# Optimization experiments

Measured on AMD Instinct MI355X. Metric: run time of the kernel, lower is better.

## Reference

```python
import jax, jax.numpy as jnp
import numpy as np

NUM_CLASSES = 21
NEGPOS_RATIO = 3
B, P = 64, 24564


def setup_inputs() -> dict:
    key = jax.random.key(0)
    ks = jax.random.split(key, 10)
    return {
        "loc_data": jax.random.normal(ks[0], (B, P, 4), jnp.float32),
        "conf_data": jax.random.normal(ks[1], (B, P, NUM_CLASSES), jnp.float32),
        "has_lp_data": jax.random.normal(ks[2], (B, P, 2), jnp.float32),
        "size_lp_data": jax.random.normal(ks[3], (B, P, 2), jnp.float32),
        "offset_data": jax.random.normal(ks[4], (B, P, 2), jnp.float32),
        "loc_t": jax.random.normal(ks[5], (B, P, 4), jnp.float32),
        "conf_t": jax.random.randint(ks[6], (B, P), 0, NUM_CLASSES, jnp.int64),
        "has_lp_t": jax.random.randint(ks[7], (B, P), 0, 2, jnp.int64),
        "size_lp_t": jax.random.normal(ks[8], (B, P, 2), jnp.float32),
        "offset_t": jax.random.normal(ks[9], (B, P, 2), jnp.float32),
    }


def _smooth_l1_sum(p, t, mask):
    # sum-reduced smooth L1 (beta=1) over elements selected by mask
    d = jnp.abs(p - t)
    l = jnp.where(d < 1.0, 0.5 * d * d, d - 0.5)
    return jnp.sum(l * mask)


def _ce_per_row(logits, labels):
    # per-row cross entropy: logsumexp(logits) - logits[label]
    lse = jax.nn.logsumexp(logits, axis=-1)
    g = jnp.take_along_axis(logits, labels[..., None], axis=-1)[..., 0]
    return lse - g


def reference(loc_data, conf_data, has_lp_data, size_lp_data, offset_data,
              loc_t, conf_t, has_lp_t, size_lp_t, offset_t):
    dt = loc_data.dtype
    num_priors = conf_data.shape[1]
    pos = conf_t > 0                                  # [B,P]
    posf = pos.astype(dt)[..., None]                  # [B,P,1]

    # localization loss over positives
    loss_l = _smooth_l1_sum(loc_data, loc_t, posf)

    # size / offset losses over positives, gated by has_lp flag
    hlp = has_lp_t.astype(dt)[..., None]              # [B,P,1]
    loss_size_lp = _smooth_l1_sum(size_lp_data * hlp, size_lp_t * hlp, posf)
    loss_offset = _smooth_l1_sum(offset_data * hlp, offset_t * hlp, posf)

    # hard negative mining on per-prior conf CE
    ce = _ce_per_row(conf_data, conf_t)               # [B,P]
    ce_mine = jnp.where(pos, 0.0, ce)
    loss_idx = jnp.argsort(-ce_mine, axis=1)          # descending sort indices
    idx_rank = jnp.argsort(loss_idx, axis=1)          # rank of each prior
    num_pos = jnp.sum(pos, axis=1, keepdims=True)     # [B,1]
    num_neg = jnp.clip(NEGPOS_RATIO * num_pos, None, num_priors - 1)
    neg = idx_rank < num_neg                          # [B,P]
    sel = (pos | neg).astype(dt)

    loss_c = jnp.sum(ce * sel)
    loss_has_lp = jnp.sum(_ce_per_row(has_lp_data, has_lp_t) * sel)

    N = jnp.sum(pos).astype(dt)
    return (loss_l / N, loss_c / N, loss_size_lp / N,
            loss_offset / N, loss_has_lp / N)
```

## Files before the change

### kernel.cpp

```cpp
#include <hip/hip_runtime.h>
#include <stdint.h>

#define NC 21
#define BATCH 64
#define PRI 24564
#define NROWS (BATCH * PRI)
#define SLABS 32
#define SLABR 768
#define GBLK (BATCH * SLABS)

typedef float f4a4 __attribute__((ext_vector_type(4), aligned(4)));

__device__ __forceinline__ float sl1f(float p, float t) {
    float d = fabsf(p - t);
    return d < 1.0f ? 0.5f * d * d : d - 0.5f;
}

__device__ __forceinline__ unsigned int f2k(float v) {
    unsigned int u = __float_as_uint(v);
    return (u & 0x80000000u) ? ~u : (u | 0x80000000u);
}

__device__ __forceinline__ unsigned int chkey(float2 ch) {
    unsigned hb = __float_as_uint(ch.y);
    return (hb & 0x80000000u) ? 0x80000000u : f2k(ch.x);
}

__device__ __forceinline__ double blockReduce(double v, double* sred) {
    #pragma unroll
    for (int off = 32; off > 0; off >>= 1)
        v += __shfl_down(v, off, 64);
    const int wid = threadIdx.x >> 6, lane = threadIdx.x & 63;
    __syncthreads();
    if (lane == 0) sred[wid] = v;
    __syncthreads();
    double r = 0.0;
    if (threadIdx.x == 0) r = sred[0] + sred[1] + sred[2] + sred[3];
    return r;
}

__global__ __launch_bounds__(256) void k_main(
    const float* __restrict__ loc_data, const float* __restrict__ conf_data,
    const float* __restrict__ has_lp_data, const float* __restrict__ size_lp_data,
    const float* __restrict__ offset_data, const float* __restrict__ loc_t,
    const int* __restrict__ conf_t, const int* __restrict__ has_lp_t,
    const float* __restrict__ size_lp_t, const float* __restrict__ offset_t,
    float2* __restrict__ ws_ch, int* __restrict__ numpos, double* __restrict__ part,
    int* __restrict__ ghist1)
{
    __shared__ int hist[4096];
    __shared__ double sred[4];
    const int tid = threadIdx.x;
    const int b = blockIdx.x >> 5, s = blockIdx.x & 31;
    for (int k = tid; k < 4096; k += 256) hist[k] = 0;
    __syncthreads();

    double aL = 0.0, aS = 0.0, aO = 0.0;
    int myp = 0;

    #pragma unroll
    for (int i = 0; i < 3; ++i) {
        const int p = s * SLABR + i * 256 + tid;
        if (p < PRI) {
            const unsigned r = (unsigned)b * PRI + p;
            const int c = conf_t[r];
            const bool pos = c > 0;
            const int hl = has_lp_t[r];

            const float* crow = conf_data + (long)r * NC;
            const f4a4* cr4 = (const f4a4*)crow;
            float row[NC];
            #pragma unroll
            for (int j = 0; j < 5; ++j) {
                f4a4 v = cr4[j];
                row[4*j+0] = v.x; row[4*j+1] = v.y; row[4*j+2] = v.z; row[4*j+3] = v.w;
            }
            row[20] = crow[20];
            float m = row[0];
            #pragma unroll
            for (int k = 1; k < NC; ++k) m = fmaxf(m, row[k]);
            float sum = 0.f;
            #pragma unroll
            for (int k = 0; k < NC; ++k) sum += __expf(row[k] - m);
            const float g = crow[c];
            const float ce = m + __logf(sum) - g;

            float4 lp = ((const float4*)loc_data)[r];
            float4 lt = ((const float4*)loc_t)[r];
            float ll = sl1f(lp.x, lt.x) + sl1f(lp.y, lt.y) + sl1f(lp.z, lt.z) + sl1f(lp.w, lt.w);
            float2 sp = ((const float2*)size_lp_data)[r];
            float2 st = ((const float2*)size_lp_t)[r];
            float ls = sl1f(sp.x, st.x) + sl1f(sp.y, st.y);
            float2 op = ((const float2*)offset_data)[r];
            float2 ot = ((const float2*)offset_t)[r];
            float lo = sl1f(op.x, ot.x) + sl1f(op.y, ot.y);
            const float pf = pos ? 1.f : 0.f;
            const float hf = (hl != 0) ? 1.f : 0.f;
            aL += (double)(pf * ll);
            aS += (double)(pf * hf * ls);
            aO += (double)(pf * hf * lo);

            float2 h2 = ((const float2*)has_lp_data)[r];
            float hm = fmaxf(h2.x, h2.y);
            float hs = __expf(h2.x - hm) + __expf(h2.y - hm);
            float hlce = fmaxf(hm + __logf(hs) - (hl != 0 ? h2.y : h2.x), 0.0f);
            unsigned hb = __float_as_uint(hlce) | (pos ? 0x80000000u : 0u);
            ws_ch[r] = make_float2(ce, __uint_as_float(hb));

            const unsigned key = pos ? 0x80000000u : f2k(ce);
            atomicAdd(&hist[key >> 20], 1);
            myp += pos ? 1 : 0;
        }
    }

    double v;
    v = blockReduce(aL, sred); if (tid == 0) part[0 * GBLK + blockIdx.x] = v;
    v = blockReduce(aS, sred); if (tid == 0) part[1 * GBLK + blockIdx.x] = v;
    v = blockReduce(aO, sred); if (tid == 0) part[2 * GBLK + blockIdx.x] = v;
    v = blockReduce((double)myp, sred);
    if (tid == 0 && v > 0.0) atomicAdd(&numpos[b], (int)(v + 0.5));

    __syncthreads();
    for (int k = tid; k < 4096; k += 256) {
        int h = hist[k];
        if (h) atomicAdd(&ghist1[(b << 12) + k], h);
    }
}

template<int NB, int ROUND>
__global__ __launch_bounds__(256) void k_pick(
    const int* __restrict__ ghist, const int* __restrict__ numpos,
    unsigned* __restrict__ prefix_io, int* __restrict__ rem_io,
    unsigned* __restrict__ selT, int* __restrict__ needed)
{
    const int b = blockIdx.x, tid = threadIdx.x;
    constexpr int CH = NB / 256;
    __shared__ int sct[256];
    __shared__ unsigned s_dig;
    __shared__ int s_rem;

    int rem;
    if (ROUND == 0) { int K = 3 * numpos[b]; if (K > PRI - 1) K = PRI - 1; rem = K; }
    else rem = rem_io[b];
    if (rem <= 0) {
        if (tid == 0) {
            prefix_io[b] = 0xFFFFFFFFu;
            rem_io[b] = 0;
            if (ROUND == 2) { selT[b] = 0xFFFFFFFFu; needed[b] = 0; }
        }
        return;
    }

    int h[CH];
    const int* g = ghist + b * NB + tid * CH;
    int ct = 0;
    #pragma unroll
    for (int j = 0; j < CH; ++j) { h[j] = g[j]; ct += h[j]; }
    sct[tid] = ct;
    __syncthreads();
    #pragma unroll
    for (int off = 1; off < 256; off <<= 1) {
        int v = (tid + off < 256) ? sct[tid + off] : 0;
        __syncthreads();
        sct[tid] += v;
        __syncthreads();
    }
    const int Safter = (tid < 255) ? sct[tid + 1] : 0;
    int cum = Safter;
    #pragma unroll
    for (int j = CH - 1; j >= 0; --j) {
        int c2 = cum + h[j];
        if (c2 >= rem && cum < rem) { s_dig = (unsigned)(tid * CH + j); s_rem = rem - cum; }
        cum = c2;
    }
    __syncthreads();
    if (tid == 0) {
        unsigned d = s_dig;
        if (ROUND == 0)      { prefix_io[b] = d;                         rem_io[b] = s_rem; }
        else if (ROUND == 1) { prefix_io[b] = (prefix_io[b] << 10) | d;  rem_io[b] = s_rem; }
        else                 { selT[b]      = (prefix_io[b] << 10) | d;  needed[b] = s_rem; }
    }
}

template<int MSHIFT, int BSHIFT>
__global__ __launch_bounds__(256) void k_hist(
    const float2* __restrict__ ws_ch, const unsigned* __restrict__ prefix_io,
    int* __restrict__ ghist)
{
    __shared__ int hist[1024];
    const int tid = threadIdx.x;
    const int b = blockIdx.x >> 5, s = blockIdx.x & 31;
    const unsigned pref = prefix_io[b];
    for (int k = tid; k < 1024; k += 256) hist[k] = 0;
    __syncthreads();
    #pragma unroll
    for (int i = 0; i < 3; ++i) {
        const int p = s * SLABR + i * 256 + tid;
        if (p < PRI) {
            unsigned key = chkey(ws_ch[(unsigned)b * PRI + p]);
            if ((key >> MSHIFT) == pref) atomicAdd(&hist[(key >> BSHIFT) & 1023], 1);
        }
    }
    __syncthreads();
    for (int k = tid; k < 1024; k += 256) {
        int h = hist[k];
        if (h) atomicAdd(&ghist[(b << 10) + k], h);
    }
}

__global__ __launch_bounds__(256) void k_cntslab(
    const float2* __restrict__ ws_ch, const unsigned* __restrict__ selT,
    int* __restrict__ scnt)
{
    __shared__ int c4[4];
    const int tid = threadIdx.x;
    const int b = blockIdx.x >> 5, s = blockIdx.x & 31;
    const unsigned T = selT[b];
    int my = 0;
    #pragma unroll
    for (int i = 0; i < 3; ++i) {
        const int p = s * SLABR + i * 256 + tid;
        if (p < PRI) my += (chkey(ws_ch[(unsigned)b * PRI + p]) == T) ? 1 : 0;
    }
    #pragma unroll
    for (int off = 32; off > 0; off >>= 1) my += __shfl_down(my, off, 64);
    if ((tid & 63) == 0) c4[tid >> 6] = my;
    __syncthreads();
    if (tid == 0) scnt[b * SLABS + s] = c4[0] + c4[1] + c4[2] + c4[3];
}

__global__ __launch_bounds__(256) void k_cut(
    const float2* __restrict__ ws_ch, const int* __restrict__ scnt,
    const unsigned* __restrict__ selT, const int* __restrict__ needed,
    int* __restrict__ cutoff)
{
    const int b = blockIdx.x, tid = threadIdx.x;
    __shared__ int s_slab, s_local, s_found;
    __shared__ int wtot[4];
    const int need = needed[b];
    if (need <= 0) { if (tid == 0) cutoff[b] = -1; return; }
    if (tid == 0) {
        int cum = 0, sl = SLABS - 1, loc = need;
        for (int s2 = 0; s2 < SLABS; ++s2) {
            int c = scnt[b * SLABS + s2];
            if (cum + c >= need) { sl = s2; loc = need - cum; break; }
            cum += c;
        }
        s_slab = sl; s_local = loc; s_found = -1;
    }
    __syncthreads();
    const unsigned T = selT[b];
    const int s = s_slab, local = s_local;
    int run = 0;
    for (int i = 0; i < 3; ++i) {
        const int p = s * SLABR + i * 256 + tid;
        bool eq = false;
        if (p < PRI) eq = (chkey(ws_ch[(unsigned)b * PRI + p]) == T);
        const unsigned long long m = __ballot(eq);
        const int lane = tid & 63, wid = tid >> 6;
        if (lane == 0) wtot[wid] = __popcll(m);
        const int mex = __popcll(m & ((1ull << lane) - 1ull));
        __syncthreads();
        int woff = 0;
        for (int w = 0; w < wid; ++w) woff += wtot[w];
        if (eq && (run + woff + mex + 1 == local)) s_found = p;
        __syncthreads();
        run += wtot[0] + wtot[1] + wtot[2] + wtot[3];
        __syncthreads();
    }
    if (tid == 0) cutoff[b] = s_found;
}

__global__ __launch_bounds__(256) void k_conf(
    const float2* __restrict__ ws_ch, const unsigned* __restrict__ selT,
    const int* __restrict__ cutoff, double* __restrict__ part)
{
    __shared__ double sred[4];
    const int tid = threadIdx.x;
    const int b = blockIdx.x >> 5, s = blockIdx.x & 31;
    const unsigned T = selT[b];
    const int cut = cutoff[b];
    double aC = 0.0, aH = 0.0;
    #pragma unroll
    for (int i = 0; i < 3; ++i) {
        const int p = s * SLABR + i * 256 + tid;
        if (p < PRI) {
            float2 ch = ws_ch[(unsigned)b * PRI + p];
            unsigned hb = __float_as_uint(ch.y);
            const bool pos = (hb >> 31) != 0;
            const unsigned key = pos ? 0x80000000u : f2k(ch.x);
            const bool sel = pos || (key > T) || (key == T && p <= cut);
            if (sel) {
                aC += (double)ch.x;
                aH += (double)__uint_as_float(hb & 0x7fffffffu);
            }
        }
    }
    double v;
    v = blockReduce(aC, sred); if (tid == 0) part[3 * GBLK + blockIdx.x] = v;
    v = blockReduce(aH, sred); if (tid == 0) part[4 * GBLK + blockIdx.x] = v;
}

__global__ __launch_bounds__(256) void k_final(
    const double* __restrict__ part, const int* __restrict__ numpos,
    float* __restrict__ out)
{
    __shared__ double sred[4];
    const int tid = threadIdx.x;
    double s[5];
    #pragma unroll
    for (int k = 0; k < 5; ++k) {
        double a = 0.0;
        for (int t = tid; t < GBLK; t += 256) a += part[k * GBLK + t];
        s[k] = blockReduce(a, sred);
    }
    double n = (tid < BATCH) ? (double)numpos[tid] : 0.0;
    n = blockReduce(n, sred);
    if (tid == 0) {
        out[0] = (float)(s[0] / n);
        out[1] = (float)(s[3] / n);
        out[2] = (float)(s[1] / n);
        out[3] = (float)(s[2] / n);
        out[4] = (float)(s[4] / n);
    }
}

extern "C" void kernel_launch(void* const* d_in, const int* in_sizes, int n_in,
                              void* d_out, int out_size, void* d_ws, size_t ws_size,
                              hipStream_t stream)
{
    const float* loc_data     = (const float*)d_in[0];
    const float* conf_data    = (const float*)d_in[1];
    const float* has_lp_data  = (const float*)d_in[2];
    const float* size_lp_data = (const float*)d_in[3];
    const float* offset_data  = (const float*)d_in[4];
    const float* loc_t        = (const float*)d_in[5];
    const int*   conf_t       = (const int*)d_in[6];
    const int*   has_lp_t     = (const int*)d_in[7];
    const float* size_lp_t    = (const float*)d_in[8];
    const float* offset_t     = (const float*)d_in[9];
    float* out = (float*)d_out;

    char* ws = (char*)d_ws;
    int* numpos        = (int*)(ws + 0);
    unsigned* selT     = (unsigned*)(ws + 256);
    int* cutoff        = (int*)(ws + 512);
    unsigned* prefix   = (unsigned*)(ws + 768);
    int* rem           = (int*)(ws + 1024);
    int* needed        = (int*)(ws + 1280);
    int* scnt          = (int*)(ws + 1536);
    double* part       = (double*)(ws + 10240);
    int* ghist1        = (int*)(ws + 92160);
    int* ghist2        = (int*)(ws + 1140736);
    int* ghist3        = (int*)(ws + 1402880);
    float2* ws_ch      = (float2*)(ws + 1665024);

    hipMemsetAsync(ws, 0, 256, stream);
    hipMemsetAsync(ws + 92160, 0, 1572864, stream);

    k_main<<<GBLK, 256, 0, stream>>>(loc_data, conf_data, has_lp_data, size_lp_data,
                                     offset_data, loc_t, conf_t, has_lp_t,
                                     size_lp_t, offset_t, ws_ch, numpos, part, ghist1);
    k_pick<4096, 0><<<BATCH, 256, 0, stream>>>(ghist1, numpos, prefix, rem, selT, needed);
    k_hist<20, 10><<<GBLK, 256, 0, stream>>>(ws_ch, prefix, ghist2);
    k_pick<1024, 1><<<BATCH, 256, 0, stream>>>(ghist2, numpos, prefix, rem, selT, needed);
    k_hist<10, 0><<<GBLK, 256, 0, stream>>>(ws_ch, prefix, ghist3);
    k_pick<1024, 2><<<BATCH, 256, 0, stream>>>(ghist3, numpos, prefix, rem, selT, needed);
    k_cntslab<<<GBLK, 256, 0, stream>>>(ws_ch, selT, scnt);
    k_cut<<<BATCH, 256, 0, stream>>>(ws_ch, scnt, selT, needed, cutoff);
    k_conf<<<GBLK, 256, 0, stream>>>(ws_ch, selT, cutoff, part);
    k_final<<<1, 256, 0, stream>>>(part, numpos, out);
}
```

Baseline: 350.0 us.

## Batch loads in main kernel, exclude positives from radix select, merge count and conf passes

The main kernel now issues all three rows' conf loads, and then all the other loads, before computing, and uses launch_bounds with 4 blocks to expose more memory-level parallelism. Positives are left out of the histograms. A new early-out handles the case where every negative is selected, so later histogram passes can skip whole batches. The separate count-slab and conf passes are merged into one pass that also accumulates the tie-key sums per slab, and the cut kernel resolves the boundary slab, which removes one full pass over the workspace. The cost is higher register pressure and a more complex tie-handling path.

```diff
diff --git a/kernel.cpp b/kernel.cpp
--- a/kernel.cpp
+++ b/kernel.cpp
@@ -8,6 +8,7 @@
 #define SLABS 32
 #define SLABR 768
 #define GBLK (BATCH * SLABS)
+#define SENT 0xFFFFFFFFu
 
 typedef float f4a4 __attribute__((ext_vector_type(4), aligned(4)));
 
@@ -39,7 +40,7 @@
     return r;
 }
 
-__global__ __launch_bounds__(256) void k_main(
+__global__ __launch_bounds__(256, 4) void k_main(
     const float* __restrict__ loc_data, const float* __restrict__ conf_data,
     const float* __restrict__ has_lp_data, const float* __restrict__ size_lp_data,
     const float* __restrict__ offset_data, const float* __restrict__ loc_t,
@@ -55,62 +56,82 @@
     for (int k = tid; k < 4096; k += 256) hist[k] = 0;
     __syncthreads();
 
+    int pr[3]; bool vld[3];
+    #pragma unroll
+    for (int i = 0; i < 3; ++i) {
+        int p = s * SLABR + i * 256 + tid;
+        vld[i] = p < PRI;
+        pr[i] = vld[i] ? p : PRI - 1;
+    }
+    const unsigned rb = (unsigned)b * PRI;
+
+    int ct[3];
+    #pragma unroll
+    for (int i = 0; i < 3; ++i) ct[i] = conf_t[rb + pr[i]];
+    f4a4 cw[3][5]; float c20[3], gg[3];
+    #pragma unroll
+    for (int i = 0; i < 3; ++i) {
+        const float* crow = conf_data + (long)(rb + pr[i]) * NC;
+        #pragma unroll
+        for (int j = 0; j < 5; ++j) cw[i][j] = ((const f4a4*)crow)[j];
+        c20[i] = crow[20];
+        gg[i] = crow[ct[i]];
+    }
+    float ce[3];
+    #pragma unroll
+    for (int i = 0; i < 3; ++i) {
+        float m = c20[i];
+        #pragma unroll
+        for (int j = 0; j < 5; ++j)
+            m = fmaxf(m, fmaxf(fmaxf(cw[i][j].x, cw[i][j].y), fmaxf(cw[i][j].z, cw[i][j].w)));
+        float sum = __expf(c20[i] - m);
+        #pragma unroll
+        for (int j = 0; j < 5; ++j)
+            sum += __expf(cw[i][j].x - m) + __expf(cw[i][j].y - m)
+                 + __expf(cw[i][j].z - m) + __expf(cw[i][j].w - m);
+        ce[i] = m + __logf(sum) - gg[i];
+    }
+    #pragma unroll
+    for (int i = 0; i < 3; ++i) {
+        if (vld[i] && ct[i] <= 0) {
+            unsigned key = f2k(ce[i]);
+            if (key != 0x80000000u) atomicAdd(&hist[key >> 20], 1);
+        }
+    }
+
+    int hl[3]; float4 lp[3], lt[3]; float2 sp2[3], st2[3], op2[3], ot2[3], hh[3];
+    #pragma unroll
+    for (int i = 0; i < 3; ++i) {
+        const unsigned r = rb + pr[i];
+        hl[i] = has_lp_t[r];
+        lp[i] = ((const float4*)loc_data)[r];
+        lt[i] = ((const float4*)loc_t)[r];
+        sp2[i] = ((const float2*)size_lp_data)[r];
+        st2[i] = ((const float2*)size_lp_t)[r];
+        op2[i] = ((const float2*)offset_data)[r];
+        ot2[i] = ((const float2*)offset_t)[r];
+        hh[i] = ((const float2*)has_lp_data)[r];
+    }
     double aL = 0.0, aS = 0.0, aO = 0.0;
     int myp = 0;
-
-    #pragma unroll
-    for (int i = 0; i < 3; ++i) {
-        const int p = s * SLABR + i * 256 + tid;
-        if (p < PRI) {
-            const unsigned r = (unsigned)b * PRI + p;
-            const int c = conf_t[r];
-            const bool pos = c > 0;
-            const int hl = has_lp_t[r];
-
-            const float* crow = conf_data + (long)r * NC;
-            const f4a4* cr4 = (const f4a4*)crow;
-            float row[NC];
-            #pragma unroll
-            for (int j = 0; j < 5; ++j) {
-                f4a4 v = cr4[j];
-                row[4*j+0] = v.x; row[4*j+1] = v.y; row[4*j+2] = v.z; row[4*j+3] = v.w;
-            }
-            row[20] = crow[20];
-            float m = row[0];
-            #pragma unroll
-            for (int k = 1; k < NC; ++k) m = fmaxf(m, row[k]);
-            float sum = 0.f;
-            #pragma unroll
-            for (int k = 0; k < NC; ++k) sum += __expf(row[k] - m);
-            const float g = crow[c];
-            const float ce = m + __logf(sum) - g;
-
-            float4 lp = ((const float4*)loc_data)[r];
-            float4 lt = ((const float4*)loc_t)[r];
-            float ll = sl1f(lp.x, lt.x) + sl1f(lp.y, lt.y) + sl1f(lp.z, lt.z) + sl1f(lp.w, lt.w);
-            float2 sp = ((const float2*)size_lp_data)[r];
-            float2 st = ((const float2*)size_lp_t)[r];
-            float ls = sl1f(sp.x, st.x) + sl1f(sp.y, st.y);
-            float2 op = ((const float2*)offset_data)[r];
-            float2 ot = ((const float2*)offset_t)[r];
-            float lo = sl1f(op.x, ot.x) + sl1f(op.y, ot.y);
-            const float pf = pos ? 1.f : 0.f;
-            const float hf = (hl != 0) ? 1.f : 0.f;
-            aL += (double)(pf * ll);
-            aS += (double)(pf * hf * ls);
-            aO += (double)(pf * hf * lo);
-
-            float2 h2 = ((const float2*)has_lp_data)[r];
-            float hm = fmaxf(h2.x, h2.y);
-            float hs = __expf(h2.x - hm) + __expf(h2.y - hm);
-            float hlce = fmaxf(hm + __logf(hs) - (hl != 0 ? h2.y : h2.x), 0.0f);
-            unsigned hb = __float_as_uint(hlce) | (pos ? 0x80000000u : 0u);
-            ws_ch[r] = make_float2(ce, __uint_as_float(hb));
-
-            const unsigned key = pos ? 0x80000000u : f2k(ce);
-            atomicAdd(&hist[key >> 20], 1);
-            myp += pos ? 1 : 0;
-        }
+    #pragma unroll
+    for (int i = 0; i < 3; ++i) {
+        const bool pos = ct[i] > 0;
+        float ll = sl1f(lp[i].x, lt[i].x) + sl1f(lp[i].y, lt[i].y)
+                 + sl1f(lp[i].z, lt[i].z) + sl1f(lp[i].w, lt[i].w);
+        float ls = sl1f(sp2[i].x, st2[i].x) + sl1f(sp2[i].y, st2[i].y);
+        float lo = sl1f(op2[i].x, ot2[i].x) + sl1f(op2[i].y, ot2[i].y);
+        const float pf = (vld[i] && pos) ? 1.f : 0.f;
+        const float hf = (hl[i] != 0) ? 1.f : 0.f;
+        aL += (double)(pf * ll);
+        aS += (double)(pf * hf * ls);
+        aO += (double)(pf * hf * lo);
+        float hm = fmaxf(hh[i].x, hh[i].y);
+        float hs = __expf(hh[i].x - hm) + __expf(hh[i].y - hm);
+        float hlce = fmaxf(hm + __logf(hs) - (hl[i] != 0 ? hh[i].y : hh[i].x), 0.0f);
+        unsigned hb = __float_as_uint(hlce) | (pos ? 0x80000000u : 0u);
+        if (vld[i]) ws_ch[rb + pr[i]] = make_float2(ce[i], __uint_as_float(hb));
+        myp += (vld[i] && pos) ? 1 : 0;
     }
 
     double v;
@@ -127,36 +148,24 @@
     }
 }
 
-template<int NB, int ROUND>
-__global__ __launch_bounds__(256) void k_pick(
-    const int* __restrict__ ghist, const int* __restrict__ numpos,
+__global__ __launch_bounds__(256) void k_pick0(
+    const int* __restrict__ ghist1, const int* __restrict__ numpos,
     unsigned* __restrict__ prefix_io, int* __restrict__ rem_io,
     unsigned* __restrict__ selT, int* __restrict__ needed)
 {
     const int b = blockIdx.x, tid = threadIdx.x;
-    constexpr int CH = NB / 256;
     __shared__ int sct[256];
     __shared__ unsigned s_dig;
     __shared__ int s_rem;
 
-    int rem;
-    if (ROUND == 0) { int K = 3 * numpos[b]; if (K > PRI - 1) K = PRI - 1; rem = K; }
-    else rem = rem_io[b];
-    if (rem <= 0) {
-        if (tid == 0) {
-            prefix_io[b] = 0xFFFFFFFFu;
-            rem_io[b] = 0;
-            if (ROUND == 2) { selT[b] = 0xFFFFFFFFu; needed[b] = 0; }
-        }
-        return;
-    }
-
-    int h[CH];
-    const int* g = ghist + b * NB + tid * CH;
-    int ct = 0;
-    #pragma unroll
-    for (int j = 0; j < CH; ++j) { h[j] = g[j]; ct += h[j]; }
-    sct[tid] = ct;
+    int K = 3 * numpos[b]; if (K > PRI - 1) K = PRI - 1;
+
+    int h[16];
+    const int* g = ghist1 + (b << 12) + tid * 16;
+    int ctn = 0;
+    #pragma unroll
+    for (int j = 0; j < 16; ++j) { h[j] = g[j]; ctn += h[j]; }
+    sct[tid] = ctn;
     __syncthreads();
     #pragma unroll
     for (int off = 1; off < 256; off <<= 1) {
@@ -165,21 +174,26 @@
         sct[tid] += v;
         __syncthreads();
     }
+    const int M = sct[0];
+
+    if (K <= 0) {
+        if (tid == 0) { selT[b] = 0xFFFFFFFFu; needed[b] = 0; rem_io[b] = 0; prefix_io[b] = SENT; }
+        return;
+    }
+    if (K > M) {
+        if (tid == 0) { selT[b] = 0x80000000u; needed[b] = K - M; rem_io[b] = 0; prefix_io[b] = SENT; }
+        return;
+    }
     const int Safter = (tid < 255) ? sct[tid + 1] : 0;
     int cum = Safter;
     #pragma unroll
-    for (int j = CH - 1; j >= 0; --j) {
+    for (int j = 15; j >= 0; --j) {
         int c2 = cum + h[j];
-        if (c2 >= rem && cum < rem) { s_dig = (unsigned)(tid * CH + j); s_rem = rem - cum; }
+        if (c2 >= K && cum < K) { s_dig = (unsigned)(tid * 16 + j); s_rem = K - cum; }
         cum = c2;
     }
     __syncthreads();
-    if (tid == 0) {
-        unsigned d = s_dig;
-        if (ROUND == 0)      { prefix_io[b] = d;                         rem_io[b] = s_rem; }
-        else if (ROUND == 1) { prefix_io[b] = (prefix_io[b] << 10) | d;  rem_io[b] = s_rem; }
-        else                 { selT[b]      = (prefix_io[b] << 10) | d;  needed[b] = s_rem; }
-    }
+    if (tid == 0) { prefix_io[b] = s_dig; rem_io[b] = s_rem; }
 }
 
 template<int MSHIFT, int BSHIFT>
@@ -187,10 +201,11 @@
     const float2* __restrict__ ws_ch, const unsigned* __restrict__ prefix_io,
     int* __restrict__ ghist)
 {
+    const int b = blockIdx.x >> 5, s = blockIdx.x & 31;
+    const unsigned pref = prefix_io[b];
+    if (pref == SENT) return;
     __shared__ int hist[1024];
     const int tid = threadIdx.x;
-    const int b = blockIdx.x >> 5, s = blockIdx.x & 31;
-    const unsigned pref = prefix_io[b];
     for (int k = tid; k < 1024; k += 256) hist[k] = 0;
     __syncthreads();
     #pragma unroll
@@ -198,7 +213,8 @@
         const int p = s * SLABR + i * 256 + tid;
         if (p < PRI) {
             unsigned key = chkey(ws_ch[(unsigned)b * PRI + p]);
-            if ((key >> MSHIFT) == pref) atomicAdd(&hist[(key >> BSHIFT) & 1023], 1);
+            if (key != 0x80000000u && (key >> MSHIFT) == pref)
+                atomicAdd(&hist[(key >> BSHIFT) & 1023], 1);
         }
     }
     __syncthreads();
@@ -208,79 +224,55 @@
     }
 }
 
-__global__ __launch_bounds__(256) void k_cntslab(
+template<int ROUND>
+__global__ __launch_bounds__(256) void k_pickR(
+    const int* __restrict__ ghist, unsigned* __restrict__ prefix_io,
+    int* __restrict__ rem_io, unsigned* __restrict__ selT, int* __restrict__ needed)
+{
+    const int b = blockIdx.x, tid = threadIdx.x;
+    const int rem = rem_io[b];
+    if (rem <= 0) return;
+    __shared__ int sct[256];
+    __shared__ unsigned s_dig;
+    __shared__ int s_rem;
+    int h[4];
+    const int* g = ghist + (b << 10) + tid * 4;
+    int ctn = 0;
+    #pragma unroll
+    for (int j = 0; j < 4; ++j) { h[j] = g[j]; ctn += h[j]; }
+    sct[tid] = ctn;
+    __syncthreads();
+    #pragma unroll
+    for (int off = 1; off < 256; off <<= 1) {
+        int v = (tid + off < 256) ? sct[tid + off] : 0;
+        __syncthreads();
+        sct[tid] += v;
+        __syncthreads();
+    }
+    const int Safter = (tid < 255) ? sct[tid + 1] : 0;
+    int cum = Safter;
+    #pragma unroll
+    for (int j = 3; j >= 0; --j) {
+        int c2 = cum + h[j];
+        if (c2 >= rem && cum < rem) { s_dig = (unsigned)(tid * 4 + j); s_rem = rem - cum; }
+        cum = c2;
+    }
+    __syncthreads();
+    if (tid == 0) {
+        if (ROUND == 1) { prefix_io[b] = (prefix_io[b] << 10) | s_dig; rem_io[b] = s_rem; }
+        else            { selT[b] = (prefix_io[b] << 10) | s_dig;      needed[b] = s_rem; }
+    }
+}
+
+__global__ __launch_bounds__(256) void k_sel2(
     const float2* __restrict__ ws_ch, const unsigned* __restrict__ selT,
-    int* __restrict__ scnt)
-{
-    __shared__ int c4[4];
-    const int tid = threadIdx.x;
-    const int b = blockIdx.x >> 5, s = blockIdx.x & 31;
-    const unsigned T = selT[b];
-    int my = 0;
-    #pragma unroll
-    for (int i = 0; i < 3; ++i) {
-        const int p = s * SLABR + i * 256 + tid;
-        if (p < PRI) my += (chkey(ws_ch[(unsigned)b * PRI + p]) == T) ? 1 : 0;
-    }
-    #pragma unroll
-    for (int off = 32; off > 0; off >>= 1) my += __shfl_down(my, off, 64);
-    if ((tid & 63) == 0) c4[tid >> 6] = my;
-    __syncthreads();
-    if (tid == 0) scnt[b * SLABS + s] = c4[0] + c4[1] + c4[2] + c4[3];
-}
-
-__global__ __launch_bounds__(256) void k_cut(
-    const float2* __restrict__ ws_ch, const int* __restrict__ scnt,
-    const unsigned* __restrict__ selT, const int* __restrict__ needed,
-    int* __restrict__ cutoff)
-{
-    const int b = blockIdx.x, tid = threadIdx.x;
-    __shared__ int s_slab, s_local, s_found;
-    __shared__ int wtot[4];
-    const int need = needed[b];
-    if (need <= 0) { if (tid == 0) cutoff[b] = -1; return; }
-    if (tid == 0) {
-        int cum = 0, sl = SLABS - 1, loc = need;
-        for (int s2 = 0; s2 < SLABS; ++s2) {
-            int c = scnt[b * SLABS + s2];
-            if (cum + c >= need) { sl = s2; loc = need - cum; break; }
-            cum += c;
-        }
-        s_slab = sl; s_local = loc; s_found = -1;
-    }
-    __syncthreads();
-    const unsigned T = selT[b];
-    const int s = s_slab, local = s_local;
-    int run = 0;
-    for (int i = 0; i < 3; ++i) {
-        const int p = s * SLABR + i * 256 + tid;
-        bool eq = false;
-        if (p < PRI) eq = (chkey(ws_ch[(unsigned)b * PRI + p]) == T);
-        const unsigned long long m = __ballot(eq);
-        const int lane = tid & 63, wid = tid >> 6;
-        if (lane == 0) wtot[wid] = __popcll(m);
-        const int mex = __popcll(m & ((1ull << lane) - 1ull));
-        __syncthreads();
-        int woff = 0;
-        for (int w = 0; w < wid; ++w) woff += wtot[w];
-        if (eq && (run + woff + mex + 1 == local)) s_found = p;
-        __syncthreads();
-        run += wtot[0] + wtot[1] + wtot[2] + wtot[3];
-        __syncthreads();
-    }
-    if (tid == 0) cutoff[b] = s_found;
-}
-
-__global__ __launch_bounds__(256) void k_conf(
-    const float2* __restrict__ ws_ch, const unsigned* __restrict__ selT,
-    const int* __restrict__ cutoff, double* __restrict__ part)
+    int* __restrict__ cntT, double* __restrict__ sums)
 {
     __shared__ double sred[4];
     const int tid = threadIdx.x;
     const int b = blockIdx.x >> 5, s = blockIdx.x & 31;
     const unsigned T = selT[b];
-    const int cut = cutoff[b];
-    double aC = 0.0, aH = 0.0;
+    double aC = 0.0, aH = 0.0, tC = 0.0, tH = 0.0, cc = 0.0;
     #pragma unroll
     for (int i = 0; i < 3; ++i) {
         const int p = s * SLABR + i * 256 + tid;
@@ -289,39 +281,124 @@
             unsigned hb = __float_as_uint(ch.y);
             const bool pos = (hb >> 31) != 0;
             const unsigned key = pos ? 0x80000000u : f2k(ch.x);
-            const bool sel = pos || (key > T) || (key == T && p <= cut);
-            if (sel) {
-                aC += (double)ch.x;
-                aH += (double)__uint_as_float(hb & 0x7fffffffu);
+            const float hlv = __uint_as_float(hb & 0x7fffffffu);
+            if (pos || key > T) { aC += (double)ch.x; aH += (double)hlv; }
+            if (key == T) {
+                cc += 1.0;
+                if (!pos) { tC += (double)ch.x; tH += (double)hlv; }
             }
         }
     }
     double v;
-    v = blockReduce(aC, sred); if (tid == 0) part[3 * GBLK + blockIdx.x] = v;
-    v = blockReduce(aH, sred); if (tid == 0) part[4 * GBLK + blockIdx.x] = v;
+    v = blockReduce(aC, sred); if (tid == 0) sums[0 * GBLK + blockIdx.x] = v;
+    v = blockReduce(aH, sred); if (tid == 0) sums[1 * GBLK + blockIdx.x] = v;
+    v = blockReduce(tC, sred); if (tid == 0) sums[2 * GBLK + blockIdx.x] = v;
+    v = blockReduce(tH, sred); if (tid == 0) sums[3 * GBLK + blockIdx.x] = v;
+    v = blockReduce(cc, sred); if (tid == 0) cntT[blockIdx.x] = (int)(v + 0.5);
+}
+
+__global__ __launch_bounds__(256) void k_cut(
+    const float2* __restrict__ ws_ch, const unsigned* __restrict__ selT,
+    const int* __restrict__ needed, const int* __restrict__ cntT,
+    const double* __restrict__ sums, double* __restrict__ lossCH)
+{
+    const int b = blockIdx.x, tid = threadIdx.x;
+    __shared__ double sred[4];
+    __shared__ int scnt_s[32];
+    __shared__ int s_sl, s_loc, s_found;
+    __shared__ int wtot[4];
+    const int need = needed[b];
+    const unsigned T = selT[b];
+
+    if (tid < 32) scnt_s[tid] = cntT[b * 32 + tid];
+    __syncthreads();
+    if (tid == 0) {
+        int sl = 32, loc = 0, cum = 0;
+        if (need > 0) {
+            for (int s2 = 0; s2 < 32; ++s2) {
+                int c2 = scnt_s[s2];
+                if (cum + c2 >= need) { sl = s2; loc = need - cum; break; }
+                cum += c2;
+            }
+        }
+        s_sl = sl; s_loc = loc; s_found = -1;
+    }
+    __syncthreads();
+    const int sl = s_sl, loc = s_loc;
+
+    double aC = 0.0, aH = 0.0;
+    if (tid < 32) {
+        aC = sums[0 * GBLK + b * 32 + tid] + (tid < sl ? sums[2 * GBLK + b * 32 + tid] : 0.0);
+        aH = sums[1 * GBLK + b * 32 + tid] + (tid < sl ? sums[3 * GBLK + b * 32 + tid] : 0.0);
+    }
+    double totC = blockReduce(aC, sred);
+    double totH = blockReduce(aH, sred);
+
+    if (sl < 32) {
+        int run = 0;
+        for (int i = 0; i < 3; ++i) {
+            const int p = sl * SLABR + i * 256 + tid;
+            bool eq = false;
+            if (p < PRI) eq = (chkey(ws_ch[(unsigned)b * PRI + p]) == T);
+            const unsigned long long m = __ballot(eq);
+            const int lane = tid & 63, wid = tid >> 6;
+            if (lane == 0) wtot[wid] = __popcll(m);
+            const int mex = __popcll(m & ((1ull << lane) - 1ull));
+            __syncthreads();
+            int woff = 0;
+            for (int w = 0; w < wid; ++w) woff += wtot[w];
+            if (eq && (run + woff + mex + 1 == loc)) s_found = p;
+            __syncthreads();
+            run += wtot[0] + wtot[1] + wtot[2] + wtot[3];
+            __syncthreads();
+        }
+        const int cutoff = s_found;
+        double pC = 0.0, pH = 0.0;
+        for (int i = 0; i < 3; ++i) {
+            const int p = sl * SLABR + i * 256 + tid;
+            if (p < PRI && p <= cutoff) {
+                float2 ch = ws_ch[(unsigned)b * PRI + p];
+                unsigned hb = __float_as_uint(ch.y);
+                const bool pos = (hb >> 31) != 0;
+                const unsigned key = pos ? 0x80000000u : f2k(ch.x);
+                if (!pos && key == T) {
+                    pC += (double)ch.x;
+                    pH += (double)__uint_as_float(hb & 0x7fffffffu);
+                }
+            }
+        }
+        double v1 = blockReduce(pC, sred);
+        double v2 = blockReduce(pH, sred);
+        if (tid == 0) { totC += v1; totH += v2; }
+    }
+    if (tid == 0) { lossCH[b] = totC; lossCH[64 + b] = totH; }
 }
 
 __global__ __launch_bounds__(256) void k_final(
     const double* __restrict__ part, const int* __restrict__ numpos,
-    float* __restrict__ out)
+    const double* __restrict__ lossCH, float* __restrict__ out)
 {
     __shared__ double sred[4];
     const int tid = threadIdx.x;
-    double s[5];
-    #pragma unroll
-    for (int k = 0; k < 5; ++k) {
+    double s[3];
+    #pragma unroll
+    for (int k = 0; k < 3; ++k) {
         double a = 0.0;
         for (int t = tid; t < GBLK; t += 256) a += part[k * GBLK + t];
         s[k] = blockReduce(a, sred);
     }
+    double lc = (tid < BATCH) ? lossCH[tid] : 0.0;
+    lc = blockReduce(lc, sred);
+    double lh = (tid < BATCH) ? lossCH[64 + tid] : 0.0;
+    lh = blockReduce(lh, sred);
     double n = (tid < BATCH) ? (double)numpos[tid] : 0.0;
     n = blockReduce(n, sred);
     if (tid == 0) {
         out[0] = (float)(s[0] / n);
-        out[1] = (float)(s[3] / n);
+        out[1] = (float)(lc / n);
         out[2] = (float)(s[1] / n);
         out[3] = (float)(s[2] / n);
-        out[4] = (float)(s[4] / n);
+        out[4] = (float)(lh / n);
     }
 }
 
@@ -342,32 +419,32 @@
     float* out = (float*)d_out;
 
     char* ws = (char*)d_ws;
-    int* numpos        = (int*)(ws + 0);
-    unsigned* selT     = (unsigned*)(ws + 256);
-    int* cutoff        = (int*)(ws + 512);
-    unsigned* prefix   = (unsigned*)(ws + 768);
-    int* rem           = (int*)(ws + 1024);
-    int* needed        = (int*)(ws + 1280);
-    int* scnt          = (int*)(ws + 1536);
-    double* part       = (double*)(ws + 10240);
-    int* ghist1        = (int*)(ws + 92160);
-    int* ghist2        = (int*)(ws + 1140736);
-    int* ghist3        = (int*)(ws + 1402880);
-    float2* ws_ch      = (float2*)(ws + 1665024);
+    int* numpos      = (int*)(ws + 0);
+    unsigned* selT   = (unsigned*)(ws + 256);
+    int* needed      = (int*)(ws + 512);
+    unsigned* prefix = (unsigned*)(ws + 768);
+    int* rem         = (int*)(ws + 1024);
+    int* cntT        = (int*)(ws + 1536);
+    double* part     = (double*)(ws + 16384);
+    double* sums     = (double*)(ws + 65536);
+    double* lossCH   = (double*)(ws + 131072);
+    int* ghist1      = (int*)(ws + 132096);
+    int* ghist2      = (int*)(ws + 1180672);
+    int* ghist3      = (int*)(ws + 1442816);
+    float2* ws_ch    = (float2*)(ws + 1704960);
 
     hipMemsetAsync(ws, 0, 256, stream);
-    hipMemsetAsync(ws + 92160, 0, 1572864, stream);
+    hipMemsetAsync(ws + 132096, 0, 1572864, stream);
 
     k_main<<<GBLK, 256, 0, stream>>>(loc_data, conf_data, has_lp_data, size_lp_data,
                                      offset_data, loc_t, conf_t, has_lp_t,
                                      size_lp_t, offset_t, ws_ch, numpos, part, ghist1);
-    k_pick<4096, 0><<<BATCH, 256, 0, stream>>>(ghist1, numpos, prefix, rem, selT, needed);
+    k_pick0<<<BATCH, 256, 0, stream>>>(ghist1, numpos, prefix, rem, selT, needed);
     k_hist<20, 10><<<GBLK, 256, 0, stream>>>(ws_ch, prefix, ghist2);
-    k_pick<1024, 1><<<BATCH, 256, 0, stream>>>(ghist2, numpos, prefix, rem, selT, needed);
+    k_pickR<1><<<BATCH, 256, 0, stream>>>(ghist2, prefix, rem, selT, needed);
     k_hist<10, 0><<<GBLK, 256, 0, stream>>>(ws_ch, prefix, ghist3);
-    k_pick<1024, 2><<<BATCH, 256, 0, stream>>>(ghist3, numpos, prefix, rem, selT, needed);
-    k_cntslab<<<GBLK, 256, 0, stream>>>(ws_ch, selT, scnt);
-    k_cut<<<BATCH, 256, 0, stream>>>(ws_ch, scnt, selT, needed, cutoff);
-    k_conf<<<GBLK, 256, 0, stream>>>(ws_ch, selT, cutoff, part);
-    k_final<<<1, 256, 0, stream>>>(part, numpos, out);
-}
+    k_pickR<2><<<BATCH, 256, 0, stream>>>(ghist3, prefix, rem, selT, needed);
+    k_sel2<<<GBLK, 256, 0, stream>>>(ws_ch, selT, cntT, sums);
+    k_cut<<<BATCH, 256, 0, stream>>>(ws_ch, selT, needed, cntT, sums, lossCH);
+    k_final<<<1, 256, 0, stream>>>(part, numpos, lossCH, out);
+}
```

Result: faster. 334.3 us (-4.5%).
